# Kernel optimization log

Measured on AMD Instinct MI355X. Metric: run time of the kernel, lower is better.

The kernel has to match this reference:

```python
import jax, jax.numpy as jnp
import numpy as np

D_MODEL = 768; D_STATE = 64; D_CONV = 7; EXPAND = 2; HEADDIM = 64; NGROUPS = 1; CHUNK = 256
D_INNER = EXPAND * D_MODEL                                      # 1536
NHEADS = D_INNER // HEADDIM                                     # 24
D_IN_PROJ = 2 * D_INNER + 2 * NGROUPS * D_STATE + 2 * NHEADS    # 3248
CONV_DIM = D_INNER + 2 * NGROUPS * D_STATE                      # 1664
BATCH, SEQLEN = 2, 4096
EPS = 1e-5


def setup_inputs() -> dict:
    key = jax.random.key(0)
    ks = jax.random.split(key, 8)
    w = lambda k, shape, s=0.02: jax.random.normal(k, shape, jnp.float32) * s
    # dt in [1e-3, 1e-1], dt_bias = softplus^{-1}(dt)
    dt0 = jnp.exp(jax.random.uniform(ks[3], (NHEADS,)) * (np.log(0.1) - np.log(0.001)) + np.log(0.001))
    return {
        "x": jax.random.normal(ks[0], (BATCH, SEQLEN, D_MODEL), jnp.float32),
        "ln_w": jnp.ones((D_MODEL,), jnp.float32),
        "ln_b": jnp.zeros((D_MODEL,), jnp.float32),
        "in_proj_w": w(ks[1], (D_IN_PROJ, D_MODEL)),
        "conv_w": w(ks[2], (CONV_DIM, D_CONV), 0.2),
        "conv_b": jnp.zeros((CONV_DIM,), jnp.float32),
        "dt_bias": dt0 + jnp.log(-jnp.expm1(-dt0)),
        "A_log": jnp.log(jax.random.uniform(ks[4], (NHEADS,), minval=1.0, maxval=16.0)),
        "D": jnp.ones((NHEADS,), jnp.float32),
        "fc_D_w": w(ks[5], (NHEADS, D_INNER)),
        "rms_w": jnp.ones((D_INNER,), jnp.float32),
        "out_proj_w": w(ks[6], (D_MODEL, D_INNER)),
    }


def _segsum(a):
    # a: (..., T) -> (..., T, T) lower-triangular segment sums, -inf above diagonal
    T = a.shape[-1]
    cs = jnp.cumsum(a, -1)
    ss = cs[..., :, None] - cs[..., None, :]
    return jnp.where(jnp.tril(jnp.ones((T, T), bool)), ss, -jnp.inf)


def _ssd(X, A, Bm, Cm):
    # Chunked SSD scan (mamba_chunk_scan_combined, D=None, z=None, ngroups=1).
    # X: (b,l,h,p) already scaled by dt; A: (b,l,h) = dt*A_head; Bm,Cm: (b,l,n)
    b, l, h, p = X.shape
    c = l // CHUNK
    X = X.reshape(b, c, CHUNK, h, p)
    A = A.reshape(b, c, CHUNK, h).transpose(0, 3, 1, 2)  # (b,h,c,l)
    Bm = Bm.reshape(b, c, CHUNK, D_STATE)
    Cm = Cm.reshape(b, c, CHUNK, D_STATE)
    A_cum = jnp.cumsum(A, -1)
    Lmat = jnp.exp(_segsum(A))                                      # (b,h,c,l,s)
    Y_diag = jnp.einsum("bcln,bcsn,bhcls,bcshp->bclhp", Cm, Bm, Lmat, X)
    decay_states = jnp.exp(A_cum[..., -1:] - A_cum)                 # (b,h,c,l)
    states = jnp.einsum("bcln,bhcl,bclhp->bchpn", Bm, decay_states, X)
    A_chunk = jnp.pad(A_cum[..., -1], ((0, 0), (0, 0), (1, 0)))     # (b,h,c+1)
    decay_chunk = jnp.exp(_segsum(A_chunk))                         # (b,h,c+1,c+1)
    all_states = jnp.concatenate([jnp.zeros_like(states[:, :1]), states], 1)
    prev = jnp.einsum("bhzc,bchpn->bzhpn", decay_chunk, all_states)[:, :-1]
    Y_off = jnp.einsum("bcln,bchpn,bhcl->bclhp", Cm, prev, jnp.exp(A_cum))
    return (Y_diag + Y_off).reshape(b, l, h, p)


def _dwconv_causal(x, w, b):
    # x: (B,L,C), w: (C,K); torch Conv1d(padding=K-1) then [:, :L] == causal conv
    xp = jnp.pad(x, ((0, 0), (D_CONV - 1, 0), (0, 0))).transpose(0, 2, 1)
    y = jax.lax.conv_general_dilated(xp, w[:, None, :], (1,), "VALID",
                                     feature_group_count=CONV_DIM,
                                     dimension_numbers=("NCH", "OIH", "NCH"))
    return y.transpose(0, 2, 1) + b


def _forward(x, ln_w, ln_b, in_proj_w, conv_w, conv_b, dt_bias, A_log, D, fc_D_w, rms_w, out_proj_w):
    B, L, _ = x.shape
    # pre-LayerNorm
    mu = jnp.mean(x, -1, keepdims=True)
    var = jnp.mean((x - mu) ** 2, -1, keepdims=True)
    u = (x - mu) * jax.lax.rsqrt(var + EPS) * ln_w + ln_b
    # input projection -> z | xBC | dt_fw,dt_bw
    zxbcdt = u @ in_proj_w.T
    z = zxbcdt[..., :D_INNER]
    xBC = zxbcdt[..., D_INNER:D_INNER + CONV_DIM]
    dt2 = zxbcdt[..., -2 * NHEADS:]
    dt = jnp.concatenate([dt2[..., :NHEADS], jnp.flip(dt2[..., NHEADS:], 1)], 0)  # (2B,L,H)
    dt = jax.nn.softplus(dt + dt_bias)
    A = -jnp.exp(A_log)
    # causal depthwise conv + SiLU
    xBC = jax.nn.silu(_dwconv_causal(xBC, conv_w, conv_b))
    xs = xBC[..., :D_INNER]
    Bm = xBC[..., D_INNER:D_INNER + D_STATE]
    Cm = xBC[..., D_INNER + D_STATE:]
    x_og = xs
    cat2 = lambda t: jnp.concatenate([t, jnp.flip(t, 1)], 0)  # fwd + reversed copy
    X = cat2(xs).reshape(2 * B, L, NHEADS, HEADDIM) * dt[..., None]
    y = _ssd(X, dt * A, cat2(Bm), cat2(Cm)).reshape(2 * B, L, D_INNER)
    # quasiseparable combine: shift each direction by one, zero the boundary
    y = jnp.roll(y, 1, axis=1).at[:, 0, :].set(0.0)
    y = y[:B] + jnp.flip(y[B:], 1)
    # data-dependent diagonal term
    Dterm = x_og @ fc_D_w.T + D                                 # (B,L,H)
    y = y + x_og * jnp.repeat(Dterm, HEADDIM, axis=-1)
    # gated RMSNorm
    y = y * jax.nn.silu(z)
    y = y * jax.lax.rsqrt(jnp.mean(y * y, -1, keepdims=True) + EPS) * rms_w
    # out projection + residual (dropout=0 -> identity)
    return y @ out_proj_w.T + x


def reference(x, ln_w, ln_b, in_proj_w, conv_w, conv_b, dt_bias, A_log, D, fc_D_w, rms_w, out_proj_w):
    return _forward(x, ln_w, ln_b, in_proj_w, conv_w, conv_b, dt_bias, A_log, D, fc_D_w, rms_w, out_proj_w)
```

## Files before the change

kernel.cpp:

```cpp
#include <hip/hip_runtime.h>
#include <hip/hip_bf16.h>
#include <cstdint>
#include <cstddef>

typedef __hip_bfloat16 bf16;
typedef __attribute__((ext_vector_type(8))) short short8;
typedef __attribute__((ext_vector_type(4))) float f32x4;

#define B_   2
#define L_   4096
#define DM_  768
#define DI_  1536
#define NH_  24
#define HD_  64
#define DS_  64
#define CH_  256
#define NC_  16
#define CD_  1664
#define DIP_ 3248
#define NPAD_ 3328
#define EPS_ 1e-5f

#define ROWS_ (B_*L_)
#define BB4_  (2*B_)

#define LDT  72

__device__ __forceinline__ float b2f(bf16 v) { return __bfloat162float(v); }
__device__ __forceinline__ bf16  f2b(float v) { return __float2bfloat16(v); }
__device__ __forceinline__ float sb2f(short s) {
    bf16 t; __builtin_memcpy(&t, &s, 2); return __bfloat162float(t);
}
__device__ __forceinline__ short f2s(float v) {
    bf16 t = __float2bfloat16(v); short s; __builtin_memcpy(&s, &t, 2); return s;
}
__device__ __forceinline__ void gl_lds16(const void* g, void* l) {
    __builtin_amdgcn_global_load_lds((const __attribute__((address_space(1))) unsigned int*)g,
                                     (__attribute__((address_space(3))) unsigned int*)l,
                                     16, 0, 0);
}

__global__ __launch_bounds__(256) void cast_f2b(const float* __restrict__ s,
                                                bf16* __restrict__ d, int n) {
    int i = (blockIdx.x * 256 + threadIdx.x) * 4;
    if (i + 3 < n) {
        float4 v = *(const float4*)(s + i);
        d[i]   = f2b(v.x); d[i+1] = f2b(v.y);
        d[i+2] = f2b(v.z); d[i+3] = f2b(v.w);
    } else {
        for (int k = i; k < n; k++) d[k] = f2b(s[k]);
    }
}

__global__ __launch_bounds__(256) void cast_pad_inproj(const float* __restrict__ s,
                                                       bf16* __restrict__ d) {
    int i = (blockIdx.x * 256 + threadIdx.x) * 4;
    const int nsrc = DIP_ * DM_;
    const int ntot = NPAD_ * DM_;
    if (i >= ntot) return;
    if (i + 3 < nsrc) {
        float4 v = *(const float4*)(s + i);
        d[i]   = f2b(v.x); d[i+1] = f2b(v.y);
        d[i+2] = f2b(v.z); d[i+3] = f2b(v.w);
    } else {
        for (int k = i; k < i + 4 && k < ntot; k++)
            d[k] = (k < nsrc) ? f2b(s[k]) : f2b(0.f);
    }
}

__global__ __launch_bounds__(256) void ln_kernel(const float* __restrict__ x,
                                                 const float* __restrict__ w,
                                                 const float* __restrict__ bb,
                                                 bf16* __restrict__ u) {
    int row = blockIdx.x, tid = threadIdx.x;
    const float* xr = x + (size_t)row * DM_;
    float v0 = xr[tid], v1 = xr[tid + 256], v2 = xr[tid + 512];
    float s = v0 + v1 + v2;
    float q = v0*v0 + v1*v1 + v2*v2;
    for (int off = 32; off > 0; off >>= 1) {
        s += __shfl_down(s, off);
        q += __shfl_down(q, off);
    }
    __shared__ float rs[4], rq[4];
    __shared__ float mean_s, rstd_s;
    int lane = tid & 63, wid = tid >> 6;
    if (!lane) { rs[wid] = s; rq[wid] = q; }
    __syncthreads();
    if (!tid) {
        float S = rs[0]+rs[1]+rs[2]+rs[3];
        float Q = rq[0]+rq[1]+rq[2]+rq[3];
        float mu = S / (float)DM_;
        float var = Q / (float)DM_ - mu*mu;
        mean_s = mu; rstd_s = rsqrtf(var + EPS_);
    }
    __syncthreads();
    float mu = mean_s, rstd = rstd_s;
    bf16* ur = u + (size_t)row * DM_;
    ur[tid]       = f2b((v0 - mu) * rstd * w[tid]       + bb[tid]);
    ur[tid + 256] = f2b((v1 - mu) * rstd * w[tid + 256] + bb[tid + 256]);
    ur[tid + 512] = f2b((v2 - mu) * rstd * w[tid + 512] + bb[tid + 512]);
}

__global__ __launch_bounds__(256) void gemm_gl_inproj(const bf16* __restrict__ A,
                                                      const bf16* __restrict__ W,
                                                      bf16* __restrict__ zbuf,
                                                      bf16* __restrict__ xbc,
                                                      float* __restrict__ dtr) {
    __shared__ short As[128 * 32];
    __shared__ short Ws[128 * 32];
    int tid = threadIdx.x;
    int wave = tid >> 6, lane = tid & 63;
    int wm = (wave >> 1) * 64, wn = (wave & 1) * 64;
    int bm = blockIdx.y * 128, bn = blockIdx.x * 128;
    int fr = lane & 15, g = lane >> 4;
    const int K = DM_;
    int srow = lane >> 2;
    int scol = ((lane & 3) ^ ((lane >> 3) & 3)) * 8;
    int rsl = (g ^ ((fr >> 1) & 3)) * 8;
    const short* Ag = (const short*)A;
    const short* Wg = (const short*)W;
    f32x4 acc[4][4] = {};
    for (int k0 = 0; k0 < K; k0 += 32) {
        __syncthreads();
        #pragma unroll
        for (int q = 0; q < 2; q++) {
            gl_lds16(Ag + (size_t)(bm + q*64 + wave*16 + srow) * K + k0 + scol,
                     &As[(q*64 + wave*16) * 32]);
            gl_lds16(Wg + (size_t)(bn + q*64 + wave*16 + srow) * K + k0 + scol,
                     &Ws[(q*64 + wave*16) * 32]);
        }
        __syncthreads();
        short8 af[4], wf[4];
        #pragma unroll
        for (int i = 0; i < 4; i++)
            af[i] = *(const short8*)&As[(wm + i*16 + fr)*32 + rsl];
        #pragma unroll
        for (int j = 0; j < 4; j++)
            wf[j] = *(const short8*)&Ws[(wn + j*16 + fr)*32 + rsl];
        #pragma unroll
        for (int i = 0; i < 4; i++)
            #pragma unroll
            for (int j = 0; j < 4; j++)
                acc[i][j] = __builtin_amdgcn_mfma_f32_16x16x32_bf16(af[i], wf[j], acc[i][j], 0, 0, 0);
    }
    int rg = (lane >> 4) * 4;
    #pragma unroll
    for (int i = 0; i < 4; i++) {
        int mrow = bm + wm + i*16 + rg;
        #pragma unroll
        for (int j = 0; j < 4; j++) {
            int ncol = bn + wn + j*16 + fr;
            #pragma unroll
            for (int r = 0; r < 4; r++) {
                float v = acc[i][j][r];
                int m = mrow + r;
                if (ncol < DI_)            zbuf[(size_t)m * DI_ + ncol] = f2b(v);
                else if (ncol < DI_ + CD_) xbc[(size_t)m * CD_ + (ncol - DI_)] = f2b(v);
                else if (ncol < DIP_)      dtr[(size_t)m * 48 + (ncol - DI_ - CD_)] = v;
            }
        }
    }
}

__global__ __launch_bounds__(256) void gemm_gl_out(const bf16* __restrict__ A,
                                                   const bf16* __restrict__ W,
                                                   const float* __restrict__ resid,
                                                   float* __restrict__ C) {
    __shared__ short As[128 * 32];
    __shared__ short Ws[128 * 32];
    int tid = threadIdx.x;
    int wave = tid >> 6, lane = tid & 63;
    int wm = (wave >> 1) * 64, wn = (wave & 1) * 64;
    int bm = blockIdx.y * 128, bn = blockIdx.x * 128;
    int fr = lane & 15, g = lane >> 4;
    const int K = DI_;
    int srow = lane >> 2;
    int scol = ((lane & 3) ^ ((lane >> 3) & 3)) * 8;
    int rsl = (g ^ ((fr >> 1) & 3)) * 8;
    const short* Ag = (const short*)A;
    const short* Wg = (const short*)W;
    f32x4 acc[4][4] = {};
    for (int k0 = 0; k0 < K; k0 += 32) {
        __syncthreads();
        #pragma unroll
        for (int q = 0; q < 2; q++) {
            gl_lds16(Ag + (size_t)(bm + q*64 + wave*16 + srow) * K + k0 + scol,
                     &As[(q*64 + wave*16) * 32]);
            gl_lds16(Wg + (size_t)(bn + q*64 + wave*16 + srow) * K + k0 + scol,
                     &Ws[(q*64 + wave*16) * 32]);
        }
        __syncthreads();
        short8 af[4], wf[4];
        #pragma unroll
        for (int i = 0; i < 4; i++)
            af[i] = *(const short8*)&As[(wm + i*16 + fr)*32 + rsl];
        #pragma unroll
        for (int j = 0; j < 4; j++)
            wf[j] = *(const short8*)&Ws[(wn + j*16 + fr)*32 + rsl];
        #pragma unroll
        for (int i = 0; i < 4; i++)
            #pragma unroll
            for (int j = 0; j < 4; j++)
                acc[i][j] = __builtin_amdgcn_mfma_f32_16x16x32_bf16(af[i], wf[j], acc[i][j], 0, 0, 0);
    }
    int rg = (lane >> 4) * 4;
    #pragma unroll
    for (int i = 0; i < 4; i++) {
        int mrow = bm + wm + i*16 + rg;
        #pragma unroll
        for (int j = 0; j < 4; j++) {
            int ncol = bn + wn + j*16 + fr;
            #pragma unroll
            for (int r = 0; r < 4; r++) {
                int m = mrow + r;
                C[(size_t)m * DM_ + ncol] = acc[i][j][r] + resid[(size_t)m * DM_ + ncol];
            }
        }
    }
}

__global__ __launch_bounds__(256) void conv_kernel(const bf16* __restrict__ xbc,
                                                   const float* __restrict__ cw,
                                                   const float* __restrict__ cb,
                                                   bf16* __restrict__ out) {
    int bid0 = blockIdx.x;
    int bid = (bid0 & 7) * 104 + (bid0 >> 3);
    int g = bid * 256 + threadIdx.x;
    int cg = g % 208;
    int tq = g / 208;
    int b = tq >> 9;
    int t0 = (tq & 511) * 8;
    int c8 = cg * 8;
    const short* src = (const short*)xbc + (size_t)(b * L_) * CD_ + c8;

    float w[7][8], acc[8][8];
    #pragma unroll
    for (int k = 0; k < 8; k++) {
        #pragma unroll
        for (int j = 0; j < 7; j++) w[j][k] = cw[(c8 + k) * 7 + j];
        float bias = cb[c8 + k];
        #pragma unroll
        for (int q = 0; q < 8; q++) acc[q][k] = bias;
    }
    #pragma unroll
    for (int m = 0; m < 14; m++) {
        int tt = t0 - 6 + m;
        float row[8];
        if (tt >= 0) {
            short8 v = *(const short8*)(src + (size_t)tt * CD_);
            #pragma unroll
            for (int k = 0; k < 8; k++) row[k] = sb2f(v[k]);
        } else {
            #pragma unroll
            for (int k = 0; k < 8; k++) row[k] = 0.f;
        }
        #pragma unroll
        for (int q = 0; q < 8; q++) {
            int j = m - q;
            if (j >= 0 && j < 7) {
                #pragma unroll
                for (int k = 0; k < 8; k++) acc[q][k] += row[k] * w[j][k];
            }
        }
    }
    #pragma unroll
    for (int q = 0; q < 8; q++) {
        short8 o;
        #pragma unroll
        for (int k = 0; k < 8; k++) {
            float a = acc[q][k];
            a = a / (1.f + __expf(-a));
            o[k] = f2s(a);
        }
        *(short8*)((short*)out + (size_t)(b * L_ + t0 + q) * CD_ + c8) = o;
    }
}

__global__ __launch_bounds__(256) void dt_kernel(const float* __restrict__ dtr,
                                                 const float* __restrict__ dt_bias,
                                                 float* __restrict__ dt4) {
    int idx = blockIdx.x * 256 + threadIdx.x;
    if (idx >= BB4_ * L_ * NH_) return;
    int h = idx % NH_;
    int t = (idx / NH_) % L_;
    int bbx = idx / (NH_ * L_);
    int bp = bbx & 1;
    float raw;
    if (bbx < 2) raw = dtr[((size_t)(bp * L_ + t)) * 48 + h];
    else         raw = dtr[((size_t)(bp * L_ + (L_ - 1 - t))) * 48 + NH_ + h];
    float v = raw + dt_bias[h];
    float dt = (v > 20.f) ? v : log1pf(__expf(v));
    dt4[idx] = dt;
}

__global__ __launch_bounds__(256) void scan_kernel(const float* __restrict__ dt4,
                                                   const float* __restrict__ A_log,
                                                   float* __restrict__ Acum) {
    int bid = blockIdx.x;
    int c  = bid % NC_;
    int h  = (bid / NC_) % NH_;
    int bbx = bid / (NC_ * NH_);
    int l = threadIdx.x;
    float Ah = -__expf(A_log[h]);
    float val = dt4[((size_t)(bbx * L_) + c * CH_ + l) * NH_ + h] * Ah;
    __shared__ float sc[256];
    sc[l] = val; __syncthreads();
    for (int off = 1; off < 256; off <<= 1) {
        float t = (l >= off) ? sc[l - off] : 0.f;
        __syncthreads();
        sc[l] += t;
        __syncthreads();
    }
    Acum[(size_t)bid * CH_ + l] = sc[l];
}

__global__ __launch_bounds__(256) void xt_kernel(const bf16* __restrict__ conv,
                                                 const float* __restrict__ dt4,
                                                 bf16* __restrict__ XT,
                                                 bf16* __restrict__ BT) {
    int bid0 = blockIdx.x;
    int bid = (bid0 & 7) * 200 + (bid0 >> 3);
    int hh = bid % 25;
    int c  = (bid / 25) % NC_;
    int bbx = bid / (25 * NC_);
    int bp = bbx & 1;
    bool flip = bbx >= 2;
    bool isB = (hh == NH_);
    int coff = isB ? DI_ : hh * HD_;
    int tid = threadIdx.x;
    __shared__ short tile[64][72];
    short* dstb = (short*)(isB ? BT : XT);
    size_t rowbase = isB ? (size_t)(bbx * 64) : (size_t)((bbx * NH_ + hh) * 64);
    for (int lt = 0; lt < 4; lt++) {
        __syncthreads();
        #pragma unroll
        for (int it = 0; it < 2; it++) {
            int li = tid + it * 256;
            int r = li >> 3, seg = (li & 7) * 8;
            int t = c * CH_ + lt * 64 + r;
            int tt = flip ? (L_ - 1 - t) : t;
            short8 v = *(const short8*)((const short*)conv + (size_t)(bp * L_ + tt) * CD_ + coff + seg);
            if (!isB) {
                float dtv = dt4[((size_t)(bbx * L_) + t) * NH_ + hh];
                #pragma unroll
                for (int k = 0; k < 8; k++) v[k] = f2s(sb2f(v[k]) * dtv);
            }
            *(short8*)&tile[r][seg] = v;
        }
        __syncthreads();
        #pragma unroll
        for (int it = 0; it < 2; it++) {
            int li = tid + it * 256;
            int p = li >> 3, seg = (li & 7) * 8;
            short8 o;
            #pragma unroll
            for (int k = 0; k < 8; k++) o[k] = tile[seg + k][p];
            *(short8*)(dstb + (rowbase + p) * L_ + c * CH_ + lt * 64 + seg) = o;
        }
    }
}

__global__ __launch_bounds__(256) void states_kernel(const bf16* __restrict__ XT,
                                                     const bf16* __restrict__ BT,
                                                     const float* __restrict__ Acum,
                                                     bf16* __restrict__ states) {
    int bid0 = blockIdx.x;
    int bid = (bid0 & 7) * 192 + (bid0 >> 3);
    int h = bid % NH_;
    int c = (bid / NH_) % NC_;
    int bbx = bid / (NH_ * NC_);
    int tid = threadIdx.x;
    int wave = tid >> 6, lane = tid & 63;
    int wr = wave >> 1, wc = wave & 1;
    int fr = lane & 15, kg = (lane >> 4) * 8, rg = (lane >> 4) * 4;
    size_t abase = ((size_t)(bbx * NH_ + h) * NC_ + c) * CH_;
    __shared__ float dec[256];
    {
        float Atot = Acum[abase + CH_ - 1];
        dec[tid] = __expf(Atot - Acum[abase + tid]);
    }
    __syncthreads();
    const short* xbase = (const short*)XT + (size_t)((bbx * NH_ + h) * 64) * L_ + c * CH_;
    const short* bbase = (const short*)BT + (size_t)(bbx * 64) * L_ + c * CH_;
    f32x4 acc[2][2] = {};
    for (int lt = 0; lt < 4; lt++) {
        #pragma unroll
        for (int ks = 0; ks < 2; ks++) {
            int l0 = lt * 64 + ks * 32 + kg;
            float d[8];
            #pragma unroll
            for (int k = 0; k < 8; k++) d[k] = dec[l0 + k];
            short8 af[2], wf[2];
            #pragma unroll
            for (int i = 0; i < 2; i++)
                af[i] = *(const short8*)(xbase + (size_t)(wr*32 + i*16 + fr) * L_ + l0);
            #pragma unroll
            for (int j = 0; j < 2; j++) {
                short8 raw = *(const short8*)(bbase + (size_t)(wc*32 + j*16 + fr) * L_ + l0);
                #pragma unroll
                for (int k = 0; k < 8; k++) raw[k] = f2s(sb2f(raw[k]) * d[k]);
                wf[j] = raw;
            }
            #pragma unroll
            for (int i = 0; i < 2; i++)
                #pragma unroll
                for (int j = 0; j < 2; j++)
                    acc[i][j] = __builtin_amdgcn_mfma_f32_16x16x32_bf16(af[i], wf[j], acc[i][j], 0, 0, 0);
        }
    }
    size_t sbase = (size_t)bid * 4096;
    #pragma unroll
    for (int i = 0; i < 2; i++)
        #pragma unroll
        for (int j = 0; j < 2; j++)
            #pragma unroll
            for (int r = 0; r < 4; r++) {
                int p = wr*32 + i*16 + rg + r;
                int n = wc*32 + j*16 + fr;
                states[sbase + p*64 + n] = f2b(acc[i][j][r]);
            }
}

__global__ __launch_bounds__(256) void chunkscan_kernel(bf16* __restrict__ sp,
                                                        const float* __restrict__ Acum) {
    int bid = blockIdx.x;
    int h = bid % NH_;
    int bbx = bid / NH_;
    int tid = threadIdx.x;
    float run[16];
    #pragma unroll
    for (int k = 0; k < 16; k++) run[k] = 0.f;
    for (int c = 0; c < NC_; c++) {
        float Tc = Acum[((size_t)(bbx * NH_ + h) * NC_ + c) * CH_ + CH_ - 1];
        float ec = __expf(Tc);
        size_t base = ((size_t)(bbx * NC_ + c) * NH_ + h) * 4096;
        #pragma unroll
        for (int k = 0; k < 16; k++) {
            size_t e = tid + k * 256;
            float sv = b2f(sp[base + e]);
            sp[base + e] = f2b(run[k]);
            run[k] = run[k] * ec + sv;
        }
    }
}

__global__ __launch_bounds__(256) void ydiag_kernel(const bf16* __restrict__ conv,
                                                    const bf16* __restrict__ XT,
                                                    const float* __restrict__ Acum,
                                                    const bf16* __restrict__ prev,
                                                    bf16* __restrict__ yf,
                                                    bf16* __restrict__ yb) {
    int bid0 = blockIdx.x;
    int bid = (bid0 & 7) * 768 + (bid0 >> 3);
    int lt = bid & 3;
    int q  = bid >> 2;
    int h  = q % NH_;
    int r2 = q / NH_;
    int c  = r2 % NC_;
    int bbx = r2 / NC_;
    int bp = bbx & 1;
    bool flip = bbx >= 2;
    int tid = threadIdx.x;
    int wave = tid >> 6, lane = tid & 63;
    int wr = wave >> 1, wc = wave & 1;
    int fr = lane & 15, kg = (lane >> 4) * 8, rg = (lane >> 4) * 4;
    size_t abase = ((size_t)(bbx * NH_ + h) * NC_ + c) * CH_;

    __shared__ short Gt[64 * LDT];

    float aLv[2][4];
    #pragma unroll
    for (int i = 0; i < 2; i++)
        #pragma unroll
        for (int r = 0; r < 4; r++)
            aLv[i][r] = Acum[abase + lt * 64 + wr*32 + i*16 + rg + r];

    short8 cf[2][2];
    #pragma unroll
    for (int i = 0; i < 2; i++) {
        int l = wr*32 + i*16 + fr;
        int t = c * CH_ + lt * 64 + l;
        int tt = flip ? (L_ - 1 - t) : t;
        const short* crow = (const short*)conv + (size_t)(bp * L_ + tt) * CD_ + DI_ + DS_;
        #pragma unroll
        for (int ks = 0; ks < 2; ks++)
            cf[i][ks] = *(const short8*)(crow + ks*32 + kg);
    }

    f32x4 acc[2][2] = {};
    size_t pbase = ((size_t)(bbx * NC_ + c) * NH_ + h) * 4096;
    #pragma unroll
    for (int ks = 0; ks < 2; ks++) {
        #pragma unroll
        for (int j = 0; j < 2; j++) {
            short8 pf = *(const short8*)((const short*)prev + pbase + (size_t)(wc*32 + j*16 + fr)*64 + ks*32 + kg);
            #pragma unroll
            for (int i = 0; i < 2; i++)
                acc[i][j] = __builtin_amdgcn_mfma_f32_16x16x32_bf16(cf[i][ks], pf, acc[i][j], 0, 0, 0);
        }
    }
    #pragma unroll
    for (int i = 0; i < 2; i++)
        #pragma unroll
        for (int r = 0; r < 4; r++) {
            float e = __expf(aLv[i][r]);
            #pragma unroll
            for (int j = 0; j < 2; j++) acc[i][j][r] *= e;
        }

    const short* xbase = (const short*)XT + (size_t)((bbx * NH_ + h) * 64) * L_ + c * CH_;

    short8 bf_c[2][2];
    float aSc[2];
    #pragma unroll
    for (int j = 0; j < 2; j++) {
        int s = wc*32 + j*16 + fr;
        int t = c * CH_ + s;
        int tt = flip ? (L_ - 1 - t) : t;
        const short* brow = (const short*)conv + (size_t)(bp * L_ + tt) * CD_ + DI_;
        #pragma unroll
        for (int ks = 0; ks < 2; ks++)
            bf_c[j][ks] = *(const short8*)(brow + ks*32 + kg);
        aSc[j] = Acum[abase + s];
    }

    for (int st = 0; st <= lt; st++) {
        short8 xf[2][2];
        #pragma unroll
        for (int j = 0; j < 2; j++)
            #pragma unroll
            for (int ks = 0; ks < 2; ks++)
                xf[j][ks] = *(const short8*)(xbase + (size_t)(wc*32 + j*16 + fr)*L_ + st*64 + ks*32 + kg);
        short8 bf_n[2][2];
        float aSn[2];
        if (st < lt) {
            #pragma unroll
            for (int j = 0; j < 2; j++) {
                int s = wc*32 + j*16 + fr;
                int t = c * CH_ + (st+1) * 64 + s;
                int tt = flip ? (L_ - 1 - t) : t;
                const short* brow = (const short*)conv + (size_t)(bp * L_ + tt) * CD_ + DI_;
                #pragma unroll
                for (int ks = 0; ks < 2; ks++)
                    bf_n[j][ks] = *(const short8*)(brow + ks*32 + kg);
                aSn[j] = Acum[abase + (st+1)*64 + s];
            }
        }
        f32x4 gacc[2][2] = {};
        #pragma unroll
        for (int ks = 0; ks < 2; ks++)
            #pragma unroll
            for (int j = 0; j < 2; j++)
                #pragma unroll
                for (int i = 0; i < 2; i++)
                    gacc[i][j] = __builtin_amdgcn_mfma_f32_16x16x32_bf16(cf[i][ks], bf_c[j][ks], gacc[i][j], 0, 0, 0);
        #pragma unroll
        for (int i = 0; i < 2; i++)
            #pragma unroll
            for (int j = 0; j < 2; j++)
                #pragma unroll
                for (int r = 0; r < 4; r++) {
                    int ll = wr*32 + i*16 + rg + r;
                    int ss = wc*32 + j*16 + fr;
                    bool valid = (st < lt) || (ll >= ss);
                    float gv = valid ? gacc[i][j][r] * __expf(aLv[i][r] - aSc[j]) : 0.f;
                    Gt[ll * LDT + ss] = f2s(gv);
                }
        __syncthreads();
        #pragma unroll
        for (int ks = 0; ks < 2; ks++) {
            short8 gf[2];
            #pragma unroll
            for (int i = 0; i < 2; i++)
                gf[i] = *(const short8*)&Gt[(wr*32 + i*16 + fr)*LDT + ks*32 + kg];
            #pragma unroll
            for (int i = 0; i < 2; i++)
                #pragma unroll
                for (int j = 0; j < 2; j++)
                    acc[i][j] = __builtin_amdgcn_mfma_f32_16x16x32_bf16(gf[i], xf[j][ks], acc[i][j], 0, 0, 0);
        }
        __syncthreads();
        if (st < lt) {
            #pragma unroll
            for (int j = 0; j < 2; j++) {
                #pragma unroll
                for (int ks = 0; ks < 2; ks++) bf_c[j][ks] = bf_n[j][ks];
                aSc[j] = aSn[j];
            }
        }
    }

    bf16* dst = flip ? yb : yf;
    #pragma unroll
    for (int i = 0; i < 2; i++)
        #pragma unroll
        for (int r = 0; r < 4; r++) {
            int l = wr*32 + i*16 + rg + r;
            int t = c * CH_ + lt * 64 + l;
            #pragma unroll
            for (int j = 0; j < 2; j++) {
                int p = wc*32 + j*16 + fr;
                dst[((size_t)(bp * L_) + t) * DI_ + h * HD_ + p] = f2b(acc[i][j][r]);
            }
        }
}

__global__ __launch_bounds__(256) void combine_kernel(const bf16* __restrict__ yf,
                                                      const bf16* __restrict__ yb,
                                                      const bf16* __restrict__ conv,
                                                      const bf16* __restrict__ zbuf,
                                                      const float* __restrict__ fcD,
                                                      const float* __restrict__ Dvec,
                                                      const float* __restrict__ rms_w,
                                                      bf16* __restrict__ ybuf) {
    int row = blockIdx.x;
    int b = row >> 12;
    int t = row & (L_ - 1);
    int tid = threadIdx.x;
    __shared__ float xog_s[DI_];
    __shared__ float dterm_s[NH_];
    __shared__ float rs[4];
    __shared__ float scale_s;
    float yv[6], xog[6], zv[6];
    const bf16* convrow = conv + (size_t)row * CD_;
    const bf16* zrow = zbuf + (size_t)row * DI_;
    const bf16* yfr = (t > 0) ? (yf + (size_t)(row - 1) * DI_) : nullptr;
    const bf16* ybr = (t < L_ - 1) ? (yb + ((size_t)(b * L_) + (L_ - 2 - t)) * DI_) : nullptr;
    #pragma unroll
    for (int k = 0; k < 6; k++) {
        int d = tid + k * 256;
        float xo = b2f(convrow[d]);
        xog[k] = xo; xog_s[d] = xo;
        zv[k] = b2f(zrow[d]);
        float y1 = yfr ? b2f(yfr[d]) : 0.f;
        float y2 = ybr ? b2f(ybr[d]) : 0.f;
        yv[k] = y1 + y2;
    }
    __syncthreads();
    int wid = tid >> 6, lane = tid & 63;
    for (int hh = 0; hh < 6; hh++) {
        int h = wid * 6 + hh;
        float s = 0.f;
        #pragma unroll
        for (int k = 0; k < 24; k++) {
            int d = lane + k * 64;
            s += xog_s[d] * fcD[(size_t)h * DI_ + d];
        }
        for (int off = 32; off > 0; off >>= 1) s += __shfl_down(s, off);
        if (!lane) dterm_s[h] = s + Dvec[h];
    }
    __syncthreads();
    float ss = 0.f;
    #pragma unroll
    for (int k = 0; k < 6; k++) {
        int d = tid + k * 256;
        int h = d >> 6;
        float y = yv[k] + xog[k] * dterm_s[h];
        float z = zv[k];
        y *= z / (1.f + __expf(-z));
        yv[k] = y;
        ss += y * y;
    }
    for (int off = 32; off > 0; off >>= 1) ss += __shfl_down(ss, off);
    if (!lane) rs[wid] = ss;
    __syncthreads();
    if (!tid) scale_s = rsqrtf((rs[0]+rs[1]+rs[2]+rs[3]) / (float)DI_ + EPS_);
    __syncthreads();
    float sc = scale_s;
    bf16* yrow = ybuf + (size_t)row * DI_;
    #pragma unroll
    for (int k = 0; k < 6; k++) {
        int d = tid + k * 256;
        yrow[d] = f2b(yv[k] * sc * rms_w[d]);
    }
}

extern "C" void kernel_launch(void* const* d_in, const int* in_sizes, int n_in,
                              void* d_out, int out_size, void* d_ws, size_t ws_size,
                              hipStream_t stream) {
    const float* x        = (const float*)d_in[0];
    const float* ln_w     = (const float*)d_in[1];
    const float* ln_b     = (const float*)d_in[2];
    const float* in_proj  = (const float*)d_in[3];
    const float* conv_w   = (const float*)d_in[4];
    const float* conv_b   = (const float*)d_in[5];
    const float* dt_bias  = (const float*)d_in[6];
    const float* A_log    = (const float*)d_in[7];
    const float* Dvec     = (const float*)d_in[8];
    const float* fc_D_w   = (const float*)d_in[9];
    const float* rms_w    = (const float*)d_in[10];
    const float* out_proj = (const float*)d_in[11];
    float* out = (float*)d_out;

    uint8_t* base = (uint8_t*)d_ws;
    size_t off = 0;
    auto alloc = [&](size_t bytes) -> void* {
        void* p = base + off;
        off += (bytes + 255) & ~(size_t)255;
        return p;
    };
    bf16*  buf_z    = (bf16*) alloc((size_t)ROWS_ * DI_ * 2);
    uint8_t* regA   = (uint8_t*)alloc((size_t)ROWS_ * CD_ * 2);
    float* buf_dtr  = (float*)alloc((size_t)ROWS_ * 48 * 4);
    bf16*  buf_conv = (bf16*) alloc((size_t)ROWS_ * CD_ * 2);
    float* buf_dt   = (float*)alloc((size_t)BB4_ * L_ * NH_ * 4);
    float* buf_acum = (float*)alloc((size_t)BB4_ * NH_ * NC_ * CH_ * 4);
    uint8_t* regB   = (uint8_t*)alloc((size_t)ROWS_ * DM_ * 4);
    bf16*  buf_yb   = (bf16*) alloc((size_t)B_ * L_ * DI_ * 2);
    bf16*  w_in_bf  = (bf16*) alloc((size_t)NPAD_ * DM_ * 2);
    bf16*  w_out_bf = (bf16*) alloc((size_t)DM_ * DI_ * 2);
    bf16*  buf_XT   = (bf16*) alloc((size_t)BB4_ * NH_ * 64 * L_ * 2);
    bf16*  buf_BT   = (bf16*) alloc((size_t)BB4_ * 64 * L_ * 2);

    bf16*  buf_xbc  = (bf16*)regA;
    bf16*  buf_sp   = (bf16*)regA;
    bf16*  buf_y    = (bf16*)regA;
    bf16*  buf_u    = (bf16*)regB;
    bf16*  buf_yf   = (bf16*)regB;

    cast_pad_inproj<<<(NPAD_ * DM_ / 4 + 255) / 256, 256, 0, stream>>>(in_proj, w_in_bf);
    cast_f2b<<<(DM_ * DI_ / 4 + 255) / 256, 256, 0, stream>>>(out_proj, w_out_bf, DM_ * DI_);
    ln_kernel<<<ROWS_, 256, 0, stream>>>(x, ln_w, ln_b, buf_u);
    gemm_gl_inproj<<<dim3(NPAD_ / 128, ROWS_ / 128), 256, 0, stream>>>(
        buf_u, w_in_bf, buf_z, buf_xbc, buf_dtr);
    conv_kernel<<<832, 256, 0, stream>>>(buf_xbc, conv_w, conv_b, buf_conv);
    dt_kernel<<<(BB4_ * L_ * NH_) / 256, 256, 0, stream>>>(buf_dtr, dt_bias, buf_dt);
    scan_kernel<<<BB4_ * NH_ * NC_, 256, 0, stream>>>(buf_dt, A_log, buf_acum);
    xt_kernel<<<BB4_ * NC_ * 25, 256, 0, stream>>>(buf_conv, buf_dt, buf_XT, buf_BT);
    states_kernel<<<BB4_ * NC_ * NH_, 256, 0, stream>>>(buf_XT, buf_BT, buf_acum, buf_sp);
    chunkscan_kernel<<<BB4_ * NH_, 256, 0, stream>>>(buf_sp, buf_acum);
    ydiag_kernel<<<BB4_ * NC_ * NH_ * 4, 256, 0, stream>>>(buf_conv, buf_XT, buf_acum, buf_sp, buf_yf, buf_yb);
    combine_kernel<<<ROWS_, 256, 0, stream>>>(buf_yf, buf_yb, buf_conv, buf_z, fc_D_w, Dvec, rms_w, buf_y);
    gemm_gl_out<<<dim3(DM_ / 128, ROWS_ / 128), 256, 0, stream>>>(
        buf_y, w_out_bf, x, out);
}
```

Before: 524.5 us.

## Keep intra-chunk G tile in registers via transposed MFMA, drop LDS round-trip

The diagonal-block SSD kernel now computes the transposed C·B^T product so that its accumulator layout directly matches the A-operand layout of a 16x16x16 bf16 MFMA. The masked, decayed G values are packed into registers and consumed without going through shared memory. This removes the LDS store/load and both __syncthreads per step. In exchange each wave recomputes the full 64-wide G row block (duplicating C·B^T work across the wc waves), loads all B rows and Acum values per step without prefetching, and uses the smaller-K MFMA for the G·X product.

Result: slower. 614.6 us (+17.2%).

```diff
diff --git a/kernel.cpp b/kernel.cpp
--- a/kernel.cpp
+++ b/kernel.cpp
@@ -5,6 +5,7 @@
 
 typedef __hip_bfloat16 bf16;
 typedef __attribute__((ext_vector_type(8))) short short8;
+typedef __attribute__((ext_vector_type(4))) short s16x4;
 typedef __attribute__((ext_vector_type(4))) float f32x4;
 
 #define B_   2
@@ -24,8 +25,6 @@
 #define ROWS_ (B_*L_)
 #define BB4_  (2*B_)
 
-#define LDT  72
-
 __device__ __forceinline__ float b2f(bf16 v) { return __bfloat162float(v); }
 __device__ __forceinline__ bf16  f2b(float v) { return __float2bfloat16(v); }
 __device__ __forceinline__ float sb2f(short s) {
@@ -38,6 +37,14 @@
     __builtin_amdgcn_global_load_lds((const __attribute__((address_space(1))) unsigned int*)g,
                                      (__attribute__((address_space(3))) unsigned int*)l,
                                      16, 0, 0);
+}
+__device__ __forceinline__ f32x4 mfma16(s16x4 a, s16x4 b, f32x4 c) {
+#if __has_builtin(__builtin_amdgcn_mfma_f32_16x16x16bf16_1k)
+    return __builtin_amdgcn_mfma_f32_16x16x16bf16_1k(a, b, c, 0, 0, 0);
+#else
+    asm("v_mfma_f32_16x16x16_bf16 %0, %1, %2, %0" : "+v"(c) : "v"(a), "v"(b));
+    return c;
+#endif
 }
 
 __global__ __launch_bounds__(256) void cast_f2b(const float* __restrict__ s,
@@ -466,14 +473,13 @@
     int fr = lane & 15, kg = (lane >> 4) * 8, rg = (lane >> 4) * 4;
     size_t abase = ((size_t)(bbx * NH_ + h) * NC_ + c) * CH_;
 
-    __shared__ short Gt[64 * LDT];
-
-    float aLv[2][4];
-    #pragma unroll
-    for (int i = 0; i < 2; i++)
-        #pragma unroll
-        for (int r = 0; r < 4; r++)
-            aLv[i][r] = Acum[abase + lt * 64 + wr*32 + i*16 + rg + r];
+    float aLv[2][4], aLl[2];
+    #pragma unroll
+    for (int i = 0; i < 2; i++) {
+        float4 t4 = *(const float4*)&Acum[abase + lt*64 + wr*32 + i*16 + rg];
+        aLv[i][0] = t4.x; aLv[i][1] = t4.y; aLv[i][2] = t4.z; aLv[i][3] = t4.w;
+        aLl[i] = Acum[abase + lt*64 + wr*32 + i*16 + fr];
+    }
 
     short8 cf[2][2];
     #pragma unroll
@@ -510,84 +516,62 @@
 
     const short* xbase = (const short*)XT + (size_t)((bbx * NH_ + h) * 64) * L_ + c * CH_;
 
-    short8 bf_c[2][2];
-    float aSc[2];
-    #pragma unroll
-    for (int j = 0; j < 2; j++) {
-        int s = wc*32 + j*16 + fr;
-        int t = c * CH_ + s;
-        int tt = flip ? (L_ - 1 - t) : t;
-        const short* brow = (const short*)conv + (size_t)(bp * L_ + tt) * CD_ + DI_;
-        #pragma unroll
-        for (int ks = 0; ks < 2; ks++)
-            bf_c[j][ks] = *(const short8*)(brow + ks*32 + kg);
-        aSc[j] = Acum[abase + s];
-    }
-
     for (int st = 0; st <= lt; st++) {
-        short8 xf[2][2];
-        #pragma unroll
-        for (int j = 0; j < 2; j++)
+        float aSv[4][4];
+        #pragma unroll
+        for (int sg = 0; sg < 4; sg++) {
+            float4 t4 = *(const float4*)&Acum[abase + st*64 + sg*16 + rg];
+            aSv[sg][0] = t4.x; aSv[sg][1] = t4.y; aSv[sg][2] = t4.z; aSv[sg][3] = t4.w;
+        }
+        short8 bfv[4][2];
+        #pragma unroll
+        for (int sg = 0; sg < 4; sg++) {
+            int s = st*64 + sg*16 + fr;
+            int t = c * CH_ + s;
+            int tt = flip ? (L_ - 1 - t) : t;
+            const short* brow = (const short*)conv + (size_t)(bp * L_ + tt) * CD_ + DI_;
             #pragma unroll
             for (int ks = 0; ks < 2; ks++)
-                xf[j][ks] = *(const short8*)(xbase + (size_t)(wc*32 + j*16 + fr)*L_ + st*64 + ks*32 + kg);
-        short8 bf_n[2][2];
-        float aSn[2];
-        if (st < lt) {
-            #pragma unroll
-            for (int j = 0; j < 2; j++) {
-                int s = wc*32 + j*16 + fr;
-                int t = c * CH_ + (st+1) * 64 + s;
-                int tt = flip ? (L_ - 1 - t) : t;
-                const short* brow = (const short*)conv + (size_t)(bp * L_ + tt) * CD_ + DI_;
+                bfv[sg][ks] = *(const short8*)(brow + ks*32 + kg);
+        }
+        s16x4 xt4[4][2];
+        #pragma unroll
+        for (int sg = 0; sg < 4; sg++)
+            #pragma unroll
+            for (int j = 0; j < 2; j++)
+                xt4[sg][j] = *(const s16x4*)(xbase + (size_t)(wc*32 + j*16 + fr)*L_ + st*64 + sg*16 + rg);
+
+        f32x4 gT[4][2] = {};
+        #pragma unroll
+        for (int sg = 0; sg < 4; sg++)
+            #pragma unroll
+            for (int i = 0; i < 2; i++)
                 #pragma unroll
                 for (int ks = 0; ks < 2; ks++)
-                    bf_n[j][ks] = *(const short8*)(brow + ks*32 + kg);
-                aSn[j] = Acum[abase + (st+1)*64 + s];
-            }
-        }
-        f32x4 gacc[2][2] = {};
-        #pragma unroll
-        for (int ks = 0; ks < 2; ks++)
-            #pragma unroll
-            for (int j = 0; j < 2; j++)
-                #pragma unroll
-                for (int i = 0; i < 2; i++)
-                    gacc[i][j] = __builtin_amdgcn_mfma_f32_16x16x32_bf16(cf[i][ks], bf_c[j][ks], gacc[i][j], 0, 0, 0);
-        #pragma unroll
-        for (int i = 0; i < 2; i++)
-            #pragma unroll
-            for (int j = 0; j < 2; j++)
+                    gT[sg][i] = __builtin_amdgcn_mfma_f32_16x16x32_bf16(bfv[sg][ks], cf[i][ks], gT[sg][i], 0, 0, 0);
+
+        s16x4 ga[4][2];
+        #pragma unroll
+        for (int sg = 0; sg < 4; sg++)
+            #pragma unroll
+            for (int i = 0; i < 2; i++) {
+                int l = lt*64 + wr*32 + i*16 + fr;
                 #pragma unroll
                 for (int r = 0; r < 4; r++) {
-                    int ll = wr*32 + i*16 + rg + r;
-                    int ss = wc*32 + j*16 + fr;
-                    bool valid = (st < lt) || (ll >= ss);
-                    float gv = valid ? gacc[i][j][r] * __expf(aLv[i][r] - aSc[j]) : 0.f;
-                    Gt[ll * LDT + ss] = f2s(gv);
+                    int s = st*64 + sg*16 + rg + r;
+                    bool valid = (st < lt) || (l >= s);
+                    float gv = valid ? gT[sg][i][r] * __expf(aLl[i] - aSv[sg][r]) : 0.f;
+                    ga[sg][i][r] = f2s(gv);
                 }
-        __syncthreads();
-        #pragma unroll
-        for (int ks = 0; ks < 2; ks++) {
-            short8 gf[2];
-            #pragma unroll
-            for (int i = 0; i < 2; i++)
-                gf[i] = *(const short8*)&Gt[(wr*32 + i*16 + fr)*LDT + ks*32 + kg];
+            }
+
+        #pragma unroll
+        for (int sg = 0; sg < 4; sg++)
             #pragma unroll
             for (int i = 0; i < 2; i++)
                 #pragma unroll
                 for (int j = 0; j < 2; j++)
-                    acc[i][j] = __builtin_amdgcn_mfma_f32_16x16x32_bf16(gf[i], xf[j][ks], acc[i][j], 0, 0, 0);
-        }
-        __syncthreads();
-        if (st < lt) {
-            #pragma unroll
-            for (int j = 0; j < 2; j++) {
-                #pragma unroll
-                for (int ks = 0; ks < 2; ks++) bf_c[j][ks] = bf_n[j][ks];
-                aSc[j] = aSn[j];
-            }
-        }
+                    acc[i][j] = mfma16(ga[sg][i], xt4[sg][j], acc[i][j]);
     }
 
     bf16* dst = flip ? yb : yf;
```
